# Performance work log

Hardware: AMD Instinct MI355X
Metric: run time of the kernel (lower is better)

The kernel has to match this reference:

```python
import jax, jax.numpy as jnp
import numpy as np

N = 50000        # number of nodes (A is [N, N] sparse adjacency)
NNZ = 1600000    # number of edges (avg degree 32)
UNITS = 64       # output feature dim


def setup_inputs() -> dict:
    key = jax.random.key(0)
    k1, k2, k3, k4 = jax.random.split(key, 4)
    rows = jax.random.randint(k1, (NNZ,), 0, N, dtype=jnp.int32)
    cols = jax.random.randint(k2, (NNZ,), 0, N, dtype=jnp.int32)
    values = jax.random.uniform(k3, (NNZ,), dtype=jnp.float32)
    # glorot-like scale for kernel of shape (N, UNITS)
    kernel = jax.random.normal(k4, (N, UNITS), dtype=jnp.float32) * np.float32(1.0 / np.sqrt(N))
    bias = jnp.zeros((UNITS,), dtype=jnp.float32)
    return {"rows": rows, "cols": cols, "values": values, "kernel": kernel, "bias": bias}


def reference(rows, cols, values, kernel, bias):
    # Faithful math of: relu(dense(A) @ kernel + bias), computed as SpMM
    # (zeros of the densified A contribute nothing, so results are identical).
    gathered = values[:, None] * kernel[cols]           # [nnz, units]
    out = jax.ops.segment_sum(gathered, rows, num_segments=N)  # [N, units]
    return jax.nn.relu(out + bias)
```

## Files before the change

kernel.cpp:

```cpp
#include <hip/hip_runtime.h>

#define UNITS 64
#define NNODES 50000
#define NBUCK 512
#define CAP 3584
#define BIN_TPB 1024
#define BIN_EPT 8
#define SPMM_TPB 1024

typedef unsigned long long u64;
typedef unsigned int u32;
typedef unsigned short u16;


__device__ __forceinline__ int rowbase_of(u32 b) {
    return (int)((b * 50000u + 511u) >> 9);
}

__global__ void gc_prep(const float* __restrict__ kf, u16* __restrict__ kb,
                        int* __restrict__ gcursor, int n4) {
    int i = blockIdx.x * blockDim.x + threadIdx.x;
    if (blockIdx.x == 0 && threadIdx.x < 256) {
        gcursor[threadIdx.x]       = threadIdx.x * CAP;
        gcursor[threadIdx.x + 256] = (threadIdx.x + 256) * CAP;
    }
    if (i >= n4) return;
    float4 f = ((const float4*)kf)[i];
    ushort4 o;
    u32 b;
    b = __float_as_uint(f.x); o.x = (u16)((b + 0x7FFFu + ((b >> 16) & 1u)) >> 16);
    b = __float_as_uint(f.y); o.y = (u16)((b + 0x7FFFu + ((b >> 16) & 1u)) >> 16);
    b = __float_as_uint(f.z); o.z = (u16)((b + 0x7FFFu + ((b >> 16) & 1u)) >> 16);
    b = __float_as_uint(f.w); o.w = (u16)((b + 0x7FFFu + ((b >> 16) & 1u)) >> 16);
    ((ushort4*)kb)[i] = o;
}

__global__ __launch_bounds__(BIN_TPB) void gc_bin(const int* __restrict__ rows,
                                                  const int* __restrict__ cols,
                                                  const float* __restrict__ values,
                                                  int* __restrict__ gcursor,
                                                  u64* __restrict__ edges, int nnz) {
    __shared__ u64 stage[BIN_TPB * BIN_EPT];
    __shared__ int hist[NBUCK];
    __shared__ int lstart[NBUCK];
    __shared__ int delta[NBUCK];
    __shared__ int wsum[8];
    int t = threadIdx.x;
    if (t < NBUCK) hist[t] = 0;
    __syncthreads();

    int blockStart = blockIdx.x * (BIN_TPB * BIN_EPT);
    int cnt = min(BIN_TPB * BIN_EPT, nnz - blockStart);

    u64 rec[BIN_EPT];
    int bk[BIN_EPT];
    int rk[BIN_EPT];
#pragma unroll
    for (int k = 0; k < BIN_EPT; ++k) {
        int idx = blockStart + k * BIN_TPB + t;
        if (idx < nnz) {
            int r = rows[idx];
            u32 c = (u32)cols[idx];
            u32 v = __float_as_uint(values[idx]);
            int b = (int)(((u32)r * 512u) / 50000u);
            int lrow = r - rowbase_of((u32)b);
            rec[k] = ((u64)v << 32) | ((u64)(u32)b << 23) | ((u64)(u32)lrow << 16) | (u64)c;
            bk[k] = b;
            rk[k] = atomicAdd(&hist[b], 1);
        } else {
            bk[k] = -1;
        }
    }
    __syncthreads();

    {
        int wid = t >> 6, ln = t & 63;
        int val = (t < NBUCK) ? hist[t] : 0;
        if (wid < 8) {
            for (int off = 1; off < 64; off <<= 1) {
                int x = __shfl_up(val, off, 64);
                if (ln >= off) val += x;
            }
            if (ln == 63) wsum[wid] = val;
        }
        __syncthreads();
        if (t == 0) {
            int s = 0;
            for (int i = 0; i < 8; ++i) { int x = wsum[i]; wsum[i] = s; s += x; }
        }
        __syncthreads();
        if (wid < 8) {
            int incl = val + wsum[wid];
            int excl = incl - hist[t];
            int h = hist[t];
            int gbase = (h > 0) ? atomicAdd(&gcursor[t], h) : 0;
            delta[t] = gbase - excl;
            lstart[t] = excl;
        }
    }
    __syncthreads();

#pragma unroll
    for (int k = 0; k < BIN_EPT; ++k) {
        if (bk[k] >= 0) stage[lstart[bk[k]] + rk[k]] = rec[k];
    }
    __syncthreads();

    for (int i = t; i < cnt; i += BIN_TPB) {
        u64 r = stage[i];
        int b = (int)((r >> 23) & 0x1FF);
        int gpos = delta[b] + i;
        if (gpos < (b + 1) * CAP) edges[gpos] = r;
    }
}

__global__ __launch_bounds__(SPMM_TPB) void gc_spmm(const u64* __restrict__ edges,
                                                    const int* __restrict__ gcursor,
                                                    const u16* __restrict__ kb,
                                                    const float* __restrict__ bias,
                                                    float* __restrict__ out) {
    __shared__ u64 stage[CAP];
    __shared__ int rhist[128];
    __shared__ int rstart[129];
    __shared__ int wsum2[2];
    int b = blockIdx.x;
    int t = threadIdx.x;
    int rowlo = rowbase_of((u32)b);
    int nrows = rowbase_of((u32)b + 1u) - rowlo;
    int count = min(gcursor[b] - b * CAP, CAP);
    const u64* eb = edges + (size_t)b * CAP;

    if (t < 128) rhist[t] = 0;
    __syncthreads();

    u64 rec[4];
    int rk[4], lr[4];
#pragma unroll
    for (int k = 0; k < 4; ++k) {
        int i = k * SPMM_TPB + t;
        if (i < count) {
            u64 r = eb[i];
            rec[k] = r;
            int l = (int)((r >> 16) & 0x7F);
            lr[k] = l;
            rk[k] = atomicAdd(&rhist[l], 1);
        } else {
            lr[k] = -1;
        }
    }
    __syncthreads();

    {
        int wid = t >> 6, ln = t & 63;
        int val = (t < 128) ? rhist[t] : 0;
        if (wid < 2) {
            for (int off = 1; off < 64; off <<= 1) {
                int x = __shfl_up(val, off, 64);
                if (ln >= off) val += x;
            }
            if (ln == 63) wsum2[wid] = val;
        }
        __syncthreads();
        if (t == 0) { int a = wsum2[0]; wsum2[0] = 0; wsum2[1] = a; }
        __syncthreads();
        if (wid < 2) rstart[t] = val + wsum2[wid] - rhist[t];
        if (t == 0) rstart[128] = count;
    }
    __syncthreads();

#pragma unroll
    for (int k = 0; k < 4; ++k) {
        if (lr[k] >= 0) stage[rstart[lr[k]] + rk[k]] = rec[k];
    }
    __syncthreads();

    int lane = t & 63;
    int half = lane >> 5;
    int ul = lane & 31;
    int w = t >> 6;
    float2 bl = ((const float2*)bias)[ul];

    for (int row = w; row < nrows; row += 16) {
        int j0 = rstart[row];
        int e  = rstart[row + 1];
        int npairs = (e - j0 + 1) >> 1;
        float ax = 0.0f, ay = 0.0f;
        for (int p = 0; p < npairs; ++p) {
            int j = j0 + 2 * p + half;
            float v = 0.0f, kx = 0.0f, ky = 0.0f;
            if (j < e) {
                u64 r = stage[j];
                u32 kk = *(const u32*)(kb + ((u32)r & 0xFFFFu) * UNITS + 2 * ul);
                kx = __uint_as_float(kk << 16);
                ky = __uint_as_float(kk & 0xFFFF0000u);
                v = __uint_as_float((u32)(r >> 32));
            }
            ax = fmaf(v, kx, ax);
            ay = fmaf(v, ky, ay);
        }
        ax += __shfl_xor(ax, 32, 64);
        ay += __shfl_xor(ay, 32, 64);
        if (half == 0) {
            float2 o;
            o.x = fmaxf(ax + bl.x, 0.0f);
            o.y = fmaxf(ay + bl.y, 0.0f);
            ((float2*)out)[(size_t)(rowlo + row) * 32 + ul] = o;
        }
    }
}

extern "C" void kernel_launch(void* const* d_in, const int* in_sizes, int n_in,
                              void* d_out, int out_size, void* d_ws, size_t ws_size,
                              hipStream_t stream) {
    const int*   rows   = (const int*)d_in[0];
    const int*   cols   = (const int*)d_in[1];
    const float* values = (const float*)d_in[2];
    const float* kern   = (const float*)d_in[3];
    const float* bias   = (const float*)d_in[4];
    float* out = (float*)d_out;

    const int nnz = in_sizes[0];

    char* ws = (char*)d_ws;
    u16* kb      = (u16*)(ws + 0);
    int* gcursor = (int*)(ws + 6400000);
    u64* edges   = (u64*)(ws + 6402048);

    int n4 = (NNODES * UNITS) / 4;
    gc_prep<<<(n4 + 255) / 256, 256, 0, stream>>>(kern, kb, gcursor, n4);

    gc_bin<<<(nnz + BIN_TPB * BIN_EPT - 1) / (BIN_TPB * BIN_EPT), BIN_TPB, 0, stream>>>(
        rows, cols, values, gcursor, edges, nnz);

    gc_spmm<<<NBUCK, SPMM_TPB, 0, stream>>>(edges, gcursor, kb, bias, out);
}
```

Baseline: 143.9 us.

## Fuse kernel bf16 prep into bin kernel, vectorize loads, widen SpMM gather

After: 116.7 us. 18.9% less time.

```diff
diff --git a/kernel.cpp b/kernel.cpp
--- a/kernel.cpp
+++ b/kernel.cpp
@@ -4,8 +4,9 @@
 #define NNODES 50000
 #define NBUCK 512
 #define CAP 3584
-#define BIN_TPB 1024
+#define BIN_TPB 512
 #define BIN_EPT 8
+#define PREP_BLOCKS 782
 #define SPMM_TPB 1024
 
 typedef unsigned long long u64;
@@ -17,54 +18,84 @@
     return (int)((b * 50000u + 511u) >> 9);
 }
 
-__global__ void gc_prep(const float* __restrict__ kf, u16* __restrict__ kb,
-                        int* __restrict__ gcursor, int n4) {
-    int i = blockIdx.x * blockDim.x + threadIdx.x;
-    if (blockIdx.x == 0 && threadIdx.x < 256) {
-        gcursor[threadIdx.x]       = threadIdx.x * CAP;
-        gcursor[threadIdx.x + 256] = (threadIdx.x + 256) * CAP;
-    }
-    if (i >= n4) return;
-    float4 f = ((const float4*)kf)[i];
-    ushort4 o;
-    u32 b;
-    b = __float_as_uint(f.x); o.x = (u16)((b + 0x7FFFu + ((b >> 16) & 1u)) >> 16);
-    b = __float_as_uint(f.y); o.y = (u16)((b + 0x7FFFu + ((b >> 16) & 1u)) >> 16);
-    b = __float_as_uint(f.z); o.z = (u16)((b + 0x7FFFu + ((b >> 16) & 1u)) >> 16);
-    b = __float_as_uint(f.w); o.w = (u16)((b + 0x7FFFu + ((b >> 16) & 1u)) >> 16);
-    ((ushort4*)kb)[i] = o;
-}
-
-__global__ __launch_bounds__(BIN_TPB) void gc_bin(const int* __restrict__ rows,
-                                                  const int* __restrict__ cols,
-                                                  const float* __restrict__ values,
-                                                  int* __restrict__ gcursor,
-                                                  u64* __restrict__ edges, int nnz) {
+__device__ __forceinline__ u16 f2bf(u32 b) {
+    return (u16)((b + 0x7FFFu + ((b >> 16) & 1u)) >> 16);
+}
+
+__global__ __launch_bounds__(BIN_TPB) void gc_bin_prep(const int* __restrict__ rows,
+                                                       const int* __restrict__ cols,
+                                                       const float* __restrict__ values,
+                                                       const float* __restrict__ kf,
+                                                       u16* __restrict__ kb,
+                                                       int* __restrict__ gcursor,
+                                                       u64* __restrict__ edges,
+                                                       int nnz, int binBlocks) {
+    int t = threadIdx.x;
+    if ((int)blockIdx.x >= binBlocks) {
+        int base = ((blockIdx.x - binBlocks) * BIN_TPB + t) * 8;
+        if (base + 8 <= NNODES * UNITS) {
+            float4 fa = ((const float4*)(kf + base))[0];
+            float4 fb = ((const float4*)(kf + base))[1];
+            ushort4 oa, ob;
+            oa.x = f2bf(__float_as_uint(fa.x)); oa.y = f2bf(__float_as_uint(fa.y));
+            oa.z = f2bf(__float_as_uint(fa.z)); oa.w = f2bf(__float_as_uint(fa.w));
+            ob.x = f2bf(__float_as_uint(fb.x)); ob.y = f2bf(__float_as_uint(fb.y));
+            ob.z = f2bf(__float_as_uint(fb.z)); ob.w = f2bf(__float_as_uint(fb.w));
+            ((ushort4*)(kb + base))[0] = oa;
+            ((ushort4*)(kb + base))[1] = ob;
+        }
+        return;
+    }
+
     __shared__ u64 stage[BIN_TPB * BIN_EPT];
     __shared__ int hist[NBUCK];
     __shared__ int lstart[NBUCK];
     __shared__ int delta[NBUCK];
     __shared__ int wsum[8];
-    int t = threadIdx.x;
-    if (t < NBUCK) hist[t] = 0;
+    hist[t] = 0;
     __syncthreads();
 
     int blockStart = blockIdx.x * (BIN_TPB * BIN_EPT);
     int cnt = min(BIN_TPB * BIN_EPT, nnz - blockStart);
+    int base_idx = blockStart + t * BIN_EPT;
+
+    int rr[BIN_EPT];
+    int cc[BIN_EPT];
+    float vv[BIN_EPT];
+    if (base_idx + BIN_EPT <= nnz) {
+        int4 ra = ((const int4*)(rows + base_idx))[0];
+        int4 rb = ((const int4*)(rows + base_idx))[1];
+        int4 ca = ((const int4*)(cols + base_idx))[0];
+        int4 cb = ((const int4*)(cols + base_idx))[1];
+        float4 va = ((const float4*)(values + base_idx))[0];
+        float4 vb = ((const float4*)(values + base_idx))[1];
+        rr[0]=ra.x; rr[1]=ra.y; rr[2]=ra.z; rr[3]=ra.w;
+        rr[4]=rb.x; rr[5]=rb.y; rr[6]=rb.z; rr[7]=rb.w;
+        cc[0]=ca.x; cc[1]=ca.y; cc[2]=ca.z; cc[3]=ca.w;
+        cc[4]=cb.x; cc[5]=cb.y; cc[6]=cb.z; cc[7]=cb.w;
+        vv[0]=va.x; vv[1]=va.y; vv[2]=va.z; vv[3]=va.w;
+        vv[4]=vb.x; vv[5]=vb.y; vv[6]=vb.z; vv[7]=vb.w;
+    } else {
+#pragma unroll
+        for (int k = 0; k < BIN_EPT; ++k) {
+            int idx = base_idx + k;
+            rr[k] = (idx < nnz) ? rows[idx] : -1;
+            cc[k] = (idx < nnz) ? cols[idx] : 0;
+            vv[k] = (idx < nnz) ? values[idx] : 0.0f;
+        }
+    }
 
     u64 rec[BIN_EPT];
     int bk[BIN_EPT];
     int rk[BIN_EPT];
 #pragma unroll
     for (int k = 0; k < BIN_EPT; ++k) {
-        int idx = blockStart + k * BIN_TPB + t;
-        if (idx < nnz) {
-            int r = rows[idx];
-            u32 c = (u32)cols[idx];
-            u32 v = __float_as_uint(values[idx]);
+        if (rr[k] >= 0) {
+            int r = rr[k];
+            u32 v = __float_as_uint(vv[k]);
             int b = (int)(((u32)r * 512u) / 50000u);
             int lrow = r - rowbase_of((u32)b);
-            rec[k] = ((u64)v << 32) | ((u64)(u32)b << 23) | ((u64)(u32)lrow << 16) | (u64)c;
+            rec[k] = ((u64)v << 32) | ((u64)(u32)b << 23) | ((u64)(u32)lrow << 16) | (u64)(u32)cc[k];
             bk[k] = b;
             rk[k] = atomicAdd(&hist[b], 1);
         } else {
@@ -75,28 +106,24 @@
 
     {
         int wid = t >> 6, ln = t & 63;
-        int val = (t < NBUCK) ? hist[t] : 0;
-        if (wid < 8) {
-            for (int off = 1; off < 64; off <<= 1) {
-                int x = __shfl_up(val, off, 64);
-                if (ln >= off) val += x;
-            }
-            if (ln == 63) wsum[wid] = val;
-        }
+        int val = hist[t];
+        for (int off = 1; off < 64; off <<= 1) {
+            int x = __shfl_up(val, off, 64);
+            if (ln >= off) val += x;
+        }
+        if (ln == 63) wsum[wid] = val;
         __syncthreads();
         if (t == 0) {
             int s = 0;
             for (int i = 0; i < 8; ++i) { int x = wsum[i]; wsum[i] = s; s += x; }
         }
         __syncthreads();
-        if (wid < 8) {
-            int incl = val + wsum[wid];
-            int excl = incl - hist[t];
-            int h = hist[t];
-            int gbase = (h > 0) ? atomicAdd(&gcursor[t], h) : 0;
-            delta[t] = gbase - excl;
-            lstart[t] = excl;
-        }
+        int incl = val + wsum[wid];
+        int excl = incl - hist[t];
+        int h = hist[t];
+        int gbase = (h > 0) ? (t * CAP + atomicAdd(&gcursor[t], h)) : 0;
+        delta[t] = gbase - excl;
+        lstart[t] = excl;
     }
     __syncthreads();
 
@@ -127,7 +154,7 @@
     int t = threadIdx.x;
     int rowlo = rowbase_of((u32)b);
     int nrows = rowbase_of((u32)b + 1u) - rowlo;
-    int count = min(gcursor[b] - b * CAP, CAP);
+    int count = min(gcursor[b], CAP);
     const u64* eb = edges + (size_t)b * CAP;
 
     if (t < 128) rhist[t] = 0;
@@ -175,36 +202,84 @@
     __syncthreads();
 
     int lane = t & 63;
-    int half = lane >> 5;
-    int ul = lane & 31;
+    int ep = lane >> 4;
+    int uq = lane & 15;
     int w = t >> 6;
-    float2 bl = ((const float2*)bias)[ul];
+    float4 bl = ((const float4*)bias)[uq];
 
     for (int row = w; row < nrows; row += 16) {
         int j0 = rstart[row];
         int e  = rstart[row + 1];
-        int npairs = (e - j0 + 1) >> 1;
-        float ax = 0.0f, ay = 0.0f;
-        for (int p = 0; p < npairs; ++p) {
-            int j = j0 + 2 * p + half;
-            float v = 0.0f, kx = 0.0f, ky = 0.0f;
-            if (j < e) {
-                u64 r = stage[j];
-                u32 kk = *(const u32*)(kb + ((u32)r & 0xFFFFu) * UNITS + 2 * ul);
-                kx = __uint_as_float(kk << 16);
-                ky = __uint_as_float(kk & 0xFFFF0000u);
+        float ax0=0.f, ay0=0.f, az0=0.f, aw0=0.f;
+        float ax1=0.f, ay1=0.f, az1=0.f, aw1=0.f;
+        float ax2=0.f, ay2=0.f, az2=0.f, aw2=0.f;
+        float ax3=0.f, ay3=0.f, az3=0.f, aw3=0.f;
+        int j = j0;
+        for (; j + 16 <= e; j += 16) {
+            u64 r0 = stage[j + 0  + ep];
+            u64 r1 = stage[j + 4  + ep];
+            u64 r2 = stage[j + 8  + ep];
+            u64 r3 = stage[j + 12 + ep];
+            u64 q0 = *(const u64*)(kb + ((u32)r0 & 0xFFFFu) * UNITS + 4 * uq);
+            u64 q1 = *(const u64*)(kb + ((u32)r1 & 0xFFFFu) * UNITS + 4 * uq);
+            u64 q2 = *(const u64*)(kb + ((u32)r2 & 0xFFFFu) * UNITS + 4 * uq);
+            u64 q3 = *(const u64*)(kb + ((u32)r3 & 0xFFFFu) * UNITS + 4 * uq);
+            float v0 = __uint_as_float((u32)(r0 >> 32));
+            float v1 = __uint_as_float((u32)(r1 >> 32));
+            float v2 = __uint_as_float((u32)(r2 >> 32));
+            float v3 = __uint_as_float((u32)(r3 >> 32));
+            u32 lo, hi;
+            lo = (u32)q0; hi = (u32)(q0 >> 32);
+            ax0 = fmaf(v0, __uint_as_float(lo << 16), ax0);
+            ay0 = fmaf(v0, __uint_as_float(lo & 0xFFFF0000u), ay0);
+            az0 = fmaf(v0, __uint_as_float(hi << 16), az0);
+            aw0 = fmaf(v0, __uint_as_float(hi & 0xFFFF0000u), aw0);
+            lo = (u32)q1; hi = (u32)(q1 >> 32);
+            ax1 = fmaf(v1, __uint_as_float(lo << 16), ax1);
+            ay1 = fmaf(v1, __uint_as_float(lo & 0xFFFF0000u), ay1);
+            az1 = fmaf(v1, __uint_as_float(hi << 16), az1);
+            aw1 = fmaf(v1, __uint_as_float(hi & 0xFFFF0000u), aw1);
+            lo = (u32)q2; hi = (u32)(q2 >> 32);
+            ax2 = fmaf(v2, __uint_as_float(lo << 16), ax2);
+            ay2 = fmaf(v2, __uint_as_float(lo & 0xFFFF0000u), ay2);
+            az2 = fmaf(v2, __uint_as_float(hi << 16), az2);
+            aw2 = fmaf(v2, __uint_as_float(hi & 0xFFFF0000u), aw2);
+            lo = (u32)q3; hi = (u32)(q3 >> 32);
+            ax3 = fmaf(v3, __uint_as_float(lo << 16), ax3);
+            ay3 = fmaf(v3, __uint_as_float(lo & 0xFFFF0000u), ay3);
+            az3 = fmaf(v3, __uint_as_float(hi << 16), az3);
+            aw3 = fmaf(v3, __uint_as_float(hi & 0xFFFF0000u), aw3);
+        }
+        for (; j < e; j += 4) {
+            int ji = j + ep;
+            float v = 0.f;
+            u64 q = 0;
+            if (ji < e) {
+                u64 r = stage[ji];
+                q = *(const u64*)(kb + ((u32)r & 0xFFFFu) * UNITS + 4 * uq);
                 v = __uint_as_float((u32)(r >> 32));
             }
-            ax = fmaf(v, kx, ax);
-            ay = fmaf(v, ky, ay);
-        }
-        ax += __shfl_xor(ax, 32, 64);
-        ay += __shfl_xor(ay, 32, 64);
-        if (half == 0) {
-            float2 o;
+            u32 lo = (u32)q, hi = (u32)(q >> 32);
+            ax0 = fmaf(v, __uint_as_float(lo << 16), ax0);
+            ay0 = fmaf(v, __uint_as_float(lo & 0xFFFF0000u), ay0);
+            az0 = fmaf(v, __uint_as_float(hi << 16), az0);
+            aw0 = fmaf(v, __uint_as_float(hi & 0xFFFF0000u), aw0);
+        }
+        float ax = (ax0 + ax1) + (ax2 + ax3);
+        float ay = (ay0 + ay1) + (ay2 + ay3);
+        float az = (az0 + az1) + (az2 + az3);
+        float aw = (aw0 + aw1) + (aw2 + aw3);
+        ax += __shfl_xor(ax, 16, 64); ax += __shfl_xor(ax, 32, 64);
+        ay += __shfl_xor(ay, 16, 64); ay += __shfl_xor(ay, 32, 64);
+        az += __shfl_xor(az, 16, 64); az += __shfl_xor(az, 32, 64);
+        aw += __shfl_xor(aw, 16, 64); aw += __shfl_xor(aw, 32, 64);
+        if (ep == 0) {
+            float4 o;
             o.x = fmaxf(ax + bl.x, 0.0f);
             o.y = fmaxf(ay + bl.y, 0.0f);
-            ((float2*)out)[(size_t)(rowlo + row) * 32 + ul] = o;
+            o.z = fmaxf(az + bl.z, 0.0f);
+            o.w = fmaxf(aw + bl.w, 0.0f);
+            ((float4*)out)[(size_t)(rowlo + row) * 16 + uq] = o;
         }
     }
 }
@@ -226,11 +301,11 @@
     int* gcursor = (int*)(ws + 6400000);
     u64* edges   = (u64*)(ws + 6402048);
 
-    int n4 = (NNODES * UNITS) / 4;
-    gc_prep<<<(n4 + 255) / 256, 256, 0, stream>>>(kern, kb, gcursor, n4);
-
-    gc_bin<<<(nnz + BIN_TPB * BIN_EPT - 1) / (BIN_TPB * BIN_EPT), BIN_TPB, 0, stream>>>(
-        rows, cols, values, gcursor, edges, nnz);
+    hipMemsetAsync(gcursor, 0, NBUCK * sizeof(int), stream);
+
+    int binBlocks = (nnz + BIN_TPB * BIN_EPT - 1) / (BIN_TPB * BIN_EPT);
+    gc_bin_prep<<<binBlocks + PREP_BLOCKS, BIN_TPB, 0, stream>>>(
+        rows, cols, values, kern, kb, gcursor, edges, nnz, binBlocks);
 
     gc_spmm<<<NBUCK, SPMM_TPB, 0, stream>>>(edges, gcursor, kb, bias, out);
 }
```
